# Kernel tuning notes

Measured on AMD Instinct MI355X. Metric: run time of the kernel, lower is better.

Reference implementation:

```python
import jax, jax.numpy as jnp
import numpy as np

N_ITER = 10
TOL = 1e-05
EPS_R = 1e-10
REG = 1e-06
F32_EPS = float(np.finfo(np.float32).eps)


def setup_inputs() -> dict:
    key = jax.random.key(0)
    K, T, F, _ = 6, 2048, 513, 2
    X = jax.random.normal(key, (K, T, F, 2), dtype=jnp.float32)
    return {"X": X}


def _aux_iva_iss(X):
    # X: (K, T, F, 2) real/imag -> complex (F, K, T)
    Xc = (X[..., 0] + 1j * X[..., 1]).astype(jnp.complex64)
    Xc = jnp.transpose(Xc, (2, 0, 1))  # (F, K, T)
    F, K, T = Xc.shape
    eyeK = jnp.eye(K, dtype=jnp.complex64)
    W = jnp.broadcast_to(eyeK, (F, K, K)).astype(jnp.complex64)  # (F, K, K)
    Xh = jnp.conj(Xc)
    done = jnp.array(False)

    for _ in range(N_ITER):
        W_old = W
        # demix: Y[f] = W[f] @ X[f]
        Y = jnp.einsum('fkm,fmt->fkt', W, Xc)
        # per-(source, frame) norms across frequency
        r = jnp.sqrt(jnp.clip(jnp.sum(jnp.abs(Y) ** 2, axis=0), EPS_R))  # (K, T)
        wt = 1.0 / jnp.clip(r, EPS_R)  # laplace contrast g'(r)/r
        # weighted covariances V[f,k] = (X_f * wt[k]) X_f^H / T + reg*I  -> (F, K, K, K)
        V = jnp.einsum('fat,kt,fbt->fkab', Xc, wt.astype(jnp.complex64), Xh) / T
        V = V + REG * eyeK
        # sequential ISS updates over target row k (vectorized over f, m)
        for k in range(K):
            wk = W[:, k, :]  # (F, K)
            wk_c = jnp.conj(wk)
            quad = jnp.einsum('fa,fmab,fb->fm', wk, V, wk_c)  # w_k V_m w_k^H
            denom = jnp.clip(quad.real, EPS_R)  # (F, K)
            num = jnp.einsum('fma,fmab,fb->fm', W, V, wk_c)  # w_m V_m w_k^H
            vk = num / denom  # (F, K)
            vk = vk.at[:, k].set((1.0 - 1.0 / jnp.sqrt(denom[:, k])).astype(jnp.complex64))
            W = W - vk[:, :, None] * wk[:, None, :]
        # emulate early-break on relative change (freeze W once converged)
        W = jnp.where(done, W_old, W)
        diff = jnp.linalg.norm((W - W_old).reshape(-1))
        rel = diff / jnp.clip(jnp.linalg.norm(W_old.reshape(-1)), F32_EPS)
        done = jnp.logical_or(done, rel < TOL)

    Y = jnp.einsum('fkm,fmt->fkt', W, Xc)  # (F, K, T)
    # ref_mic == 0 -> no projection-back rescaling
    Y_out = jnp.transpose(Y, (1, 2, 0))  # (K, T, F)
    return jnp.stack([Y_out.real, Y_out.imag], axis=-1)  # (K, T, F, 2)


def reference(X):
    return _aux_iva_iss(X)
```

## Files before the change

### kernel.cpp

```cpp
#include <hip/hip_runtime.h>
#include <hip/hip_bf16.h>
#include <math.h>

#define T_DIM 2048
#define F_DIM 513
#define N_ITER 10

#define OFF_W0   0
#define OFF_W1   36936
#define OFF_FLG  73872
#define OFF_RA0  73892
#define OFF_RA1  86180
#define OFF_VP   98468

typedef __attribute__((ext_vector_type(8))) short bf16x8;
typedef __attribute__((ext_vector_type(4))) float f32x4;

static __device__ inline unsigned pack2bf(float a, float b) {
    union { __hip_bfloat16 h; unsigned short u; } ca, cb;
    ca.h = __float2bfloat16(a);
    cb.h = __float2bfloat16(b);
    return (unsigned)ca.u | ((unsigned)cb.u << 16);
}

static __device__ inline void scatterV(float* V6, int e, float sum) {
    if (e < 6) {
        V6[(e * 6 + e) * 2]     = sum + 1e-6f;
        V6[(e * 6 + e) * 2 + 1] = 0.f;
    } else if (e < 21) {
        int p = e - 6;
        int a = (p < 1) ? 1 : (p < 3) ? 2 : (p < 6) ? 3 : (p < 10) ? 4 : 5;
        int b = p - a * (a - 1) / 2;
        V6[(a * 6 + b) * 2] = sum;
        V6[(b * 6 + a) * 2] = sum;
    } else {
        int p = e - 21;
        int a = (p < 1) ? 1 : (p < 3) ? 2 : (p < 6) ? 3 : (p < 10) ? 4 : 5;
        int b = p - a * (a - 1) / 2;
        V6[(a * 6 + b) * 2 + 1] =  sum;
        V6[(b * 6 + a) * 2 + 1] = -sum;
    }
}

static __device__ inline bool flag_frozen(const float* flg) {
    float rel = sqrtf(flg[0]) / fmaxf(sqrtf(flg[1]), 1.1920929e-07f);
    return rel < 1e-5f;
}

__global__ __launch_bounds__(256) void transp(const float2* __restrict__ X,
                                              float2* __restrict__ Xt,
                                              float* __restrict__ ws) {
    const int fb  = blockIdx.x + 64 * (blockIdx.y + 17 * blockIdx.z);
    const int tid = threadIdx.x;
    if (fb < 73) {
        int idx = fb * 256 + tid;
        if (idx < F_DIM * 36) {
            int e = idx % 36;
            ws[OFF_W0 + 2 * idx]     = ((e / 6) == (e % 6)) ? 1.0f : 0.0f;
            ws[OFF_W0 + 2 * idx + 1] = 0.0f;
        }
    } else if (fb == 73) {
        if (tid < 20) ws[OFF_FLG + tid] = 0.0f;
    } else if (fb < 122) {
        int idx = (fb - 74) * 256 + tid;
        if (idx < 12288) ws[OFF_RA0 + idx] = 0.0f;
    }

    __shared__ float2 tile[32][33];
    const int k  = blockIdx.z;
    const int t0 = blockIdx.x * 32;
    const int f0 = blockIdx.y * 32;
    const int tx = tid & 31, ty = tid >> 5;
#pragma unroll
    for (int j = 0; j < 4; ++j) {
        int t = t0 + ty + j * 8;
        int f = f0 + tx;
        if (f < F_DIM) tile[ty + j * 8][tx] = X[((size_t)k * T_DIM + t) * F_DIM + f];
    }
    __syncthreads();
#pragma unroll
    for (int j = 0; j < 4; ++j) {
        int f = f0 + ty + j * 8;
        int t = t0 + tx;
        if (f < F_DIM) Xt[((size_t)f * 6 + k) * T_DIM + t] = tile[tx][ty + j * 8];
    }
}

__global__ __launch_bounds__(256) void passA1C(const float2* __restrict__ Xt,
                                               float* __restrict__ ws,
                                               const float* __restrict__ flgIn,
                                               float* __restrict__ flgOut,
                                               const float* __restrict__ wOld,
                                               float* __restrict__ wNew,
                                               float* __restrict__ r2acc,
                                               int do_iss, int gate_en) {
    __shared__ float Wl[16][72];
    __shared__ float VL[16][432];
    const int tid = threadIdx.x, wv = tid >> 6, lane = tid & 63;
    const int tc = blockIdx.x, fc = blockIdx.y;

    const bool frozen = gate_en ? flag_frozen(flgIn) : false;

    const int fl = wv * 4 + (lane >> 4);
    const int f  = fc * 16 + fl;
    const int m  = lane & 15;
    const bool act = (f < F_DIM) && (m < 6);

    if (do_iss == 0) {
        if (act) {
            const float* Wp = wOld + ((size_t)f * 36 + m * 6) * 2;
#pragma unroll
            for (int a = 0; a < 6; ++a) {
                Wl[fl][(m * 6 + a) * 2]     = Wp[2 * a];
                Wl[fl][(m * 6 + a) * 2 + 1] = Wp[2 * a + 1];
            }
        }
    } else if (frozen) {
        if (act) {
            const float* Wp = wOld + ((size_t)f * 36 + m * 6) * 2;
            float* Wq = wNew + ((size_t)f * 36 + m * 6) * 2;
#pragma unroll
            for (int a = 0; a < 6; ++a) {
                Wq[2 * a] = Wp[2 * a]; Wq[2 * a + 1] = Wp[2 * a + 1];
            }
        }
        if (tc == 0 && m == 0 && f < F_DIM) atomicAdd(&flgOut[1], 1.0f);
    } else {
        if (f < F_DIM) {
            const float* vp = ws + OFF_VP + (size_t)f * 4 * 216;
            for (int v = m; v < 216; v += 16) {
                float sum = (vp[v] + vp[216 + v] + vp[432 + v] + vp[648 + v]) * (1.0f / (float)T_DIM);
                scatterV(&VL[fl][(v / 36) * 72], v % 36, sum);
            }
        }
        __syncthreads();
        float w6[6][2], wo6[6][2];
#pragma unroll
        for (int a = 0; a < 6; ++a) { w6[a][0] = 0.f; w6[a][1] = 0.f; wo6[a][0] = 0.f; wo6[a][1] = 0.f; }
        if (act) {
            const float* Wp = wOld + ((size_t)f * 36 + m * 6) * 2;
#pragma unroll
            for (int a = 0; a < 6; ++a) {
                w6[a][0] = Wp[2 * a]; w6[a][1] = Wp[2 * a + 1];
                wo6[a][0] = w6[a][0]; wo6[a][1] = w6[a][1];
            }
        }
        const float2* Vm = (const float2*)&VL[fl][0];
        for (int kk = 0; kk < 6; ++kk) {
            float wk[6][2];
#pragma unroll
            for (int a = 0; a < 6; ++a) {
                wk[a][0] = __shfl(w6[a][0], kk, 16);
                wk[a][1] = __shfl(w6[a][1], kk, 16);
            }
            if (act) {
                float t6[6][2];
#pragma unroll
                for (int a = 0; a < 6; ++a) {
                    float tr = 0.f, ti = 0.f;
#pragma unroll
                    for (int b = 0; b < 6; ++b) {
                        float2 vv = Vm[m * 36 + a * 6 + b];
                        tr += vv.x * wk[b][0] + vv.y * wk[b][1];
                        ti += vv.y * wk[b][0] - vv.x * wk[b][1];
                    }
                    t6[a][0] = tr; t6[a][1] = ti;
                }
                float quad = 0.f, nr = 0.f, ni = 0.f;
#pragma unroll
                for (int a = 0; a < 6; ++a) {
                    quad += wk[a][0] * t6[a][0] - wk[a][1] * t6[a][1];
                    nr   += w6[a][0] * t6[a][0] - w6[a][1] * t6[a][1];
                    ni   += w6[a][0] * t6[a][1] + w6[a][1] * t6[a][0];
                }
                float denom = fmaxf(quad, 1e-10f);
                float vkr, vki;
                if (m == kk) { vkr = 1.0f - 1.0f / sqrtf(denom); vki = 0.0f; }
                else { float inv = 1.0f / denom; vkr = nr * inv; vki = ni * inv; }
#pragma unroll
                for (int a = 0; a < 6; ++a) {
                    w6[a][0] -= vkr * wk[a][0] - vki * wk[a][1];
                    w6[a][1] -= vkr * wk[a][1] + vki * wk[a][0];
                }
            }
        }
        float d2 = 0.f, o2 = 0.f;
        if (act) {
            float* Wq = wNew + ((size_t)f * 36 + m * 6) * 2;
#pragma unroll
            for (int a = 0; a < 6; ++a) {
                Wq[2 * a] = w6[a][0]; Wq[2 * a + 1] = w6[a][1];
                Wl[fl][(m * 6 + a) * 2] = w6[a][0]; Wl[fl][(m * 6 + a) * 2 + 1] = w6[a][1];
                float dr = w6[a][0] - wo6[a][0], di = w6[a][1] - wo6[a][1];
                d2 += dr * dr + di * di;
                o2 += wo6[a][0] * wo6[a][0] + wo6[a][1] * wo6[a][1];
            }
        }
#pragma unroll
        for (int d = 1; d < 8; d <<= 1) {
            d2 += __shfl_xor(d2, d);
            o2 += __shfl_xor(o2, d);
        }
        if (tc == 0 && m == 0 && f < F_DIM) {
            atomicAdd(&flgOut[0], d2);
            atomicAdd(&flgOut[1], o2);
        }
    }
    __syncthreads();
    if (do_iss && frozen) return;

    float* r2s = &VL[0][0];
    const int t2 = tc * 128 + lane * 2;
    float acc[6][2];
#pragma unroll
    for (int k = 0; k < 6; ++k) { acc[k][0] = 0.f; acc[k][1] = 0.f; }
#pragma unroll
    for (int i = 0; i < 4; ++i) {
        const int ff = fc * 16 + wv * 4 + i;
        if (ff < F_DIM) {
            const float2* xf = Xt + (size_t)ff * 6 * T_DIM;
            float4 x4[6];
#pragma unroll
            for (int mm = 0; mm < 6; ++mm)
                x4[mm] = *(const float4*)(xf + (size_t)mm * T_DIM + t2);
            const float* wrow = Wl[wv * 4 + i];
#pragma unroll
            for (int k = 0; k < 6; ++k) {
                float y0r = 0.f, y0i = 0.f, y1r = 0.f, y1i = 0.f;
#pragma unroll
                for (int mm = 0; mm < 6; ++mm) {
                    float wr = wrow[(k * 6 + mm) * 2], wi = wrow[(k * 6 + mm) * 2 + 1];
                    y0r += wr * x4[mm].x - wi * x4[mm].y;
                    y0i += wr * x4[mm].y + wi * x4[mm].x;
                    y1r += wr * x4[mm].z - wi * x4[mm].w;
                    y1i += wr * x4[mm].w + wi * x4[mm].z;
                }
                acc[k][0] += y0r * y0r + y0i * y0i;
                acc[k][1] += y1r * y1r + y1i * y1i;
            }
        }
    }
    __syncthreads();
#pragma unroll
    for (int k = 0; k < 6; ++k) {
        r2s[(wv * 6 + k) * 128 + lane * 2]     = acc[k][0];
        r2s[(wv * 6 + k) * 128 + lane * 2 + 1] = acc[k][1];
    }
    __syncthreads();
    for (int v = tid; v < 768; v += 256) {
        int k = v >> 7, l = v & 127;
        float s = r2s[(0 * 6 + k) * 128 + l] + r2s[(1 * 6 + k) * 128 + l]
                + r2s[(2 * 6 + k) * 128 + l] + r2s[(3 * 6 + k) * 128 + l];
        atomicAdd(&r2acc[k * T_DIM + tc * 128 + l], s);
    }
}

__global__ __launch_bounds__(384) void passB(const float2* __restrict__ Xt,
                                             float* __restrict__ ws,
                                             const float* __restrict__ flgIn,
                                             const float* __restrict__ r2in,
                                             float* __restrict__ r2zero,
                                             int gate_en) {
    __shared__ __align__(16) char plane[16 * 528];
    __shared__ __align__(16) float gbuf[6][256];
    const int tid = threadIdx.x, wv = tid >> 6, lane = tid & 63;
    const int f = blockIdx.x, tq = blockIdx.y;

    if (gate_en && flag_frozen(flgIn)) return;

    {
        int bb = (f * 4 + tq) * 6;
#pragma unroll
        for (int i = 0; i < 6; ++i) {
            int idx = bb + i;
            if (idx < 12288) r2zero[idx] = 0.f;
        }
    }

    const float2* xb = Xt + (size_t)f * 6 * T_DIM;

    for (int i = tid; i < 528; i += 384) ((unsigned*)(plane + 12 * 528))[i] = 0;

    f32x4 acc0 = {0.f, 0.f, 0.f, 0.f};
    f32x4 acc1 = {0.f, 0.f, 0.f, 0.f};
    const int rc = lane & 15;
    const int G  = lane >> 4;
    const char* pu = plane + rc * 528 + G * 16;
    const float* gk = &gbuf[wv][0] + G * 8;

    for (int c = 0; c < 2; ++c) {
        const int t0 = tq * 512 + c * 256;
        __syncthreads();
        for (int i = tid; i < 1536; i += 384) {
            int kk = i >> 8, toff = i & 255;
            float s = r2in[kk * T_DIM + t0 + toff];
            float r = sqrtf(fmaxf(s, 1e-10f));
            gbuf[kk][toff] = 1.0f / fmaxf(r, 1e-10f);
        }
        for (int it = tid; it < 768; it += 384) {
            int mm = it >> 7, q = it & 127;
            float4 xv = *(const float4*)(xb + (size_t)mm * T_DIM + t0 + 2 * q);
            *(unsigned*)(plane + mm * 528 + 4 * q)       = pack2bf(xv.x, xv.z);
            *(unsigned*)(plane + (6 + mm) * 528 + 4 * q) = pack2bf(xv.y, xv.w);
        }
        __syncthreads();
#pragma unroll
        for (int s = 0; s < 8; ++s) {
            bf16x8 b = *(const bf16x8*)(pu + s * 64);
            f32x4 gA = *(const f32x4*)(gk + s * 32);
            f32x4 gB = *(const f32x4*)(gk + s * 32 + 4);
            const unsigned* bu = (const unsigned*)&b;
            bf16x8 a;
            unsigned* au = (unsigned*)&a;
            au[0] = pack2bf(__uint_as_float(bu[0] << 16) * gA[0],
                            __uint_as_float(bu[0] & 0xffff0000u) * gA[1]);
            au[1] = pack2bf(__uint_as_float(bu[1] << 16) * gA[2],
                            __uint_as_float(bu[1] & 0xffff0000u) * gA[3]);
            au[2] = pack2bf(__uint_as_float(bu[2] << 16) * gB[0],
                            __uint_as_float(bu[2] & 0xffff0000u) * gB[1]);
            au[3] = pack2bf(__uint_as_float(bu[3] << 16) * gB[2],
                            __uint_as_float(bu[3] & 0xffff0000u) * gB[3]);
            if (s & 1) acc1 = __builtin_amdgcn_mfma_f32_16x16x32_bf16(a, b, acc1, 0, 0, 0);
            else       acc0 = __builtin_amdgcn_mfma_f32_16x16x32_bf16(a, b, acc0, 0, 0, 0);
        }
    }
    __syncthreads();

    float* S = (float*)plane;
    {
        float* Sk = S + wv * 256;
#pragma unroll
        for (int r = 0; r < 4; ++r)
            Sk[(4 * G + r) * 16 + rc] = acc0[r] + acc1[r];
    }
    __syncthreads();

    if (tid < 216) {
        const int kk = tid / 36, e = tid % 36;
        const float* Sk = S + kk * 256;
        float val;
        if (e < 6) {
            val = Sk[e * 16 + e] + Sk[(6 + e) * 16 + (6 + e)];
        } else if (e < 21) {
            int p = e - 6;
            int a = (p < 1) ? 1 : (p < 3) ? 2 : (p < 6) ? 3 : (p < 10) ? 4 : 5;
            int b = p - a * (a - 1) / 2;
            val = Sk[a * 16 + b] + Sk[(6 + a) * 16 + (6 + b)];
        } else {
            int p = e - 21;
            int a = (p < 1) ? 1 : (p < 3) ? 2 : (p < 6) ? 3 : (p < 10) ? 4 : 5;
            int b = p - a * (a - 1) / 2;
            val = Sk[(6 + a) * 16 + b] - Sk[a * 16 + (6 + b)];
        }
        ws[OFF_VP + ((size_t)f * 4 + tq) * 216 + tid] = val;
    }
}

__global__ __launch_bounds__(64) void passC(float* __restrict__ ws,
                                            const float* __restrict__ flgIn,
                                            const float* __restrict__ wOld,
                                            float* __restrict__ wNew) {
    __shared__ float VL[432];
    const int f = blockIdx.x;
    const int lane = threadIdx.x;
    if (flag_frozen(flgIn)) {
        for (int v = lane; v < 72; v += 64)
            wNew[(size_t)f * 72 + v] = wOld[(size_t)f * 72 + v];
        return;
    }
    {
        const float* vp = ws + OFF_VP + (size_t)f * 4 * 216;
        for (int v = lane; v < 216; v += 64) {
            float sum = (vp[v] + vp[216 + v] + vp[432 + v] + vp[648 + v]) * (1.0f / (float)T_DIM);
            scatterV(&VL[(v / 36) * 72], v % 36, sum);
        }
    }
    __syncthreads();

    const int m = lane;
    const bool act = (m < 6);
    float w6[6][2];
#pragma unroll
    for (int a = 0; a < 6; ++a) { w6[a][0] = 0.f; w6[a][1] = 0.f; }
    if (act) {
        const float* Wp = wOld + ((size_t)f * 36 + m * 6) * 2;
#pragma unroll
        for (int a = 0; a < 6; ++a) {
            w6[a][0] = Wp[2 * a]; w6[a][1] = Wp[2 * a + 1];
        }
    }
    const float2* Vm = (const float2*)VL;
    for (int kk = 0; kk < 6; ++kk) {
        float wk[6][2];
#pragma unroll
        for (int a = 0; a < 6; ++a) {
            wk[a][0] = __shfl(w6[a][0], kk);
            wk[a][1] = __shfl(w6[a][1], kk);
        }
        if (act) {
            float t6[6][2];
#pragma unroll
            for (int a = 0; a < 6; ++a) {
                float tr = 0.f, ti = 0.f;
#pragma unroll
                for (int b = 0; b < 6; ++b) {
                    float2 vv = Vm[m * 36 + a * 6 + b];
                    tr += vv.x * wk[b][0] + vv.y * wk[b][1];
                    ti += vv.y * wk[b][0] - vv.x * wk[b][1];
                }
                t6[a][0] = tr; t6[a][1] = ti;
            }
            float quad = 0.f, nr = 0.f, ni = 0.f;
#pragma unroll
            for (int a = 0; a < 6; ++a) {
                quad += wk[a][0] * t6[a][0] - wk[a][1] * t6[a][1];
                nr   += w6[a][0] * t6[a][0] - w6[a][1] * t6[a][1];
                ni   += w6[a][0] * t6[a][1] + w6[a][1] * t6[a][0];
            }
            float denom = fmaxf(quad, 1e-10f);
            float vkr, vki;
            if (m == kk) { vkr = 1.0f - 1.0f / sqrtf(denom); vki = 0.0f; }
            else { float inv = 1.0f / denom; vkr = nr * inv; vki = ni * inv; }
#pragma unroll
            for (int a = 0; a < 6; ++a) {
                w6[a][0] -= vkr * wk[a][0] - vki * wk[a][1];
                w6[a][1] -= vkr * wk[a][1] + vki * wk[a][0];
            }
        }
    }
    if (act) {
        float* Wq = wNew + ((size_t)f * 36 + m * 6) * 2;
#pragma unroll
        for (int a = 0; a < 6; ++a) {
            Wq[2 * a] = w6[a][0]; Wq[2 * a + 1] = w6[a][1];
        }
    }
}

__global__ __launch_bounds__(256) void finalY(const float2* __restrict__ X,
                                              const float* __restrict__ ws,
                                              float2* __restrict__ out) {
    const int f  = blockIdx.y * 256 + threadIdx.x;
    const int t0 = blockIdx.x * 4;
    if (f >= F_DIM) return;
    const float2* Wf = (const float2*)(ws + OFF_W0) + (size_t)f * 36;
    float2 w[36];
#pragma unroll
    for (int i = 0; i < 36; ++i) w[i] = Wf[i];
#pragma unroll
    for (int tl = 0; tl < 4; ++tl) {
        int t = t0 + tl;
        float2 x[6];
#pragma unroll
        for (int m = 0; m < 6; ++m) x[m] = X[((size_t)m * T_DIM + t) * F_DIM + f];
#pragma unroll
        for (int k = 0; k < 6; ++k) {
            float yr = 0.f, yi = 0.f;
#pragma unroll
            for (int m = 0; m < 6; ++m) {
                float2 wk = w[k * 6 + m];
                yr += wk.x * x[m].x - wk.y * x[m].y;
                yi += wk.x * x[m].y + wk.y * x[m].x;
            }
            out[((size_t)k * T_DIM + t) * F_DIM + f] = make_float2(yr, yi);
        }
    }
}

extern "C" void kernel_launch(void* const* d_in, const int* in_sizes, int n_in,
                              void* d_out, int out_size, void* d_ws, size_t ws_size,
                              hipStream_t stream) {
    (void)in_sizes; (void)n_in; (void)out_size; (void)ws_size;
    const float2* X = (const float2*)d_in[0];
    float* ws = (float*)d_ws;
    float2* out = (float2*)d_out;
    float2* Xt = out;

    float* W[2]  = {ws + OFF_W0,  ws + OFF_W1};
    float* RA[2] = {ws + OFF_RA0, ws + OFF_RA1};
    float* FLG   = ws + OFF_FLG;

    transp<<<dim3(64, 17, 6), 256, 0, stream>>>(X, Xt, ws);
    for (int it = 0; it < N_ITER; ++it) {
        const float* wOld = (it == 0) ? W[0] : W[(it + 1) & 1];
        float* wNew = W[it & 1];
        const float* gIn = (it >= 2) ? FLG + 2 * (it - 2) : FLG;
        float* gOut      = (it >= 1) ? FLG + 2 * (it - 1) : FLG + 18;
        passA1C<<<dim3(16, 33), 256, 0, stream>>>(Xt, ws, gIn, gOut, wOld, wNew,
                                                  RA[it & 1], it > 0, it >= 2);
        const float* gB = (it >= 1) ? FLG + 2 * (it - 1) : FLG;
        passB<<<dim3(F_DIM, 4), 384, 0, stream>>>(Xt, ws, gB,
                                                  RA[it & 1], RA[(it + 1) & 1], it >= 1);
    }
    passC<<<F_DIM, 64, 0, stream>>>(ws, FLG + 16, W[1], W[0]);
    finalY<<<dim3(T_DIM / 4, 3), 256, 0, stream>>>(X, ws, out);
}
```

Measured before the change: 575.2 us.

## Split ISS update out of demix pass into separate per-frequency kernel

Moves the per-frequency ISS update, which each of the 16 time-chunk blocks in the fused kernel computed redundantly, into a separate small kernel with one block per frequency. The demix/norm kernel then only loads the updated W and, with LDS reduced to the W tile and reduction buffer, may fit more blocks per CU. The final ISS pass reuses the same kernel. This removes redundant ISS arithmetic and lowers LDS pressure, at the cost of an extra kernel launch per iteration and a global round trip for W.

```diff
diff --git a/kernel.cpp b/kernel.cpp
--- a/kernel.cpp
+++ b/kernel.cpp
@@ -86,130 +86,123 @@
     }
 }
 
-__global__ __launch_bounds__(256) void passA1C(const float2* __restrict__ Xt,
-                                               float* __restrict__ ws,
-                                               const float* __restrict__ flgIn,
-                                               float* __restrict__ flgOut,
-                                               const float* __restrict__ wOld,
-                                               float* __restrict__ wNew,
-                                               float* __restrict__ r2acc,
-                                               int do_iss, int gate_en) {
+__global__ __launch_bounds__(64) void passI(float* __restrict__ ws,
+                                            const float* __restrict__ flgIn,
+                                            float* __restrict__ flgOut,
+                                            const float* __restrict__ wOld,
+                                            float* __restrict__ wNew,
+                                            int gate_en) {
+    __shared__ float VL[432];
+    const int f = blockIdx.x;
+    const int lane = threadIdx.x;
+    if (gate_en && flag_frozen(flgIn)) {
+        for (int v = lane; v < 72; v += 64)
+            wNew[(size_t)f * 72 + v] = wOld[(size_t)f * 72 + v];
+        if (lane == 0) atomicAdd(&flgOut[1], 1.0f);
+        return;
+    }
+    {
+        const float* vp = ws + OFF_VP + (size_t)f * 4 * 216;
+        for (int v = lane; v < 216; v += 64) {
+            float sum = (vp[v] + vp[216 + v] + vp[432 + v] + vp[648 + v]) * (1.0f / (float)T_DIM);
+            scatterV(&VL[(v / 36) * 72], v % 36, sum);
+        }
+    }
+    __syncthreads();
+
+    const int m = lane;
+    const bool act = (m < 6);
+    float w6[6][2], wo6[6][2];
+#pragma unroll
+    for (int a = 0; a < 6; ++a) { w6[a][0] = 0.f; w6[a][1] = 0.f; wo6[a][0] = 0.f; wo6[a][1] = 0.f; }
+    if (act) {
+        const float* Wp = wOld + ((size_t)f * 36 + m * 6) * 2;
+#pragma unroll
+        for (int a = 0; a < 6; ++a) {
+            w6[a][0] = Wp[2 * a]; w6[a][1] = Wp[2 * a + 1];
+            wo6[a][0] = w6[a][0]; wo6[a][1] = w6[a][1];
+        }
+    }
+    const float2* Vm = (const float2*)VL;
+    for (int kk = 0; kk < 6; ++kk) {
+        float wk[6][2];
+#pragma unroll
+        for (int a = 0; a < 6; ++a) {
+            wk[a][0] = __shfl(w6[a][0], kk);
+            wk[a][1] = __shfl(w6[a][1], kk);
+        }
+        if (act) {
+            float t6[6][2];
+#pragma unroll
+            for (int a = 0; a < 6; ++a) {
+                float tr = 0.f, ti = 0.f;
+#pragma unroll
+                for (int b = 0; b < 6; ++b) {
+                    float2 vv = Vm[m * 36 + a * 6 + b];
+                    tr += vv.x * wk[b][0] + vv.y * wk[b][1];
+                    ti += vv.y * wk[b][0] - vv.x * wk[b][1];
+                }
+                t6[a][0] = tr; t6[a][1] = ti;
+            }
+            float quad = 0.f, nr = 0.f, ni = 0.f;
+#pragma unroll
+            for (int a = 0; a < 6; ++a) {
+                quad += wk[a][0] * t6[a][0] - wk[a][1] * t6[a][1];
+                nr   += w6[a][0] * t6[a][0] - w6[a][1] * t6[a][1];
+                ni   += w6[a][0] * t6[a][1] + w6[a][1] * t6[a][0];
+            }
+            float denom = fmaxf(quad, 1e-10f);
+            float vkr, vki;
+            if (m == kk) { vkr = 1.0f - 1.0f / sqrtf(denom); vki = 0.0f; }
+            else { float inv = 1.0f / denom; vkr = nr * inv; vki = ni * inv; }
+#pragma unroll
+            for (int a = 0; a < 6; ++a) {
+                w6[a][0] -= vkr * wk[a][0] - vki * wk[a][1];
+                w6[a][1] -= vkr * wk[a][1] + vki * wk[a][0];
+            }
+        }
+    }
+    float d2 = 0.f, o2 = 0.f;
+    if (act) {
+        float* Wq = wNew + ((size_t)f * 36 + m * 6) * 2;
+#pragma unroll
+        for (int a = 0; a < 6; ++a) {
+            Wq[2 * a] = w6[a][0]; Wq[2 * a + 1] = w6[a][1];
+            float dr = w6[a][0] - wo6[a][0], di = w6[a][1] - wo6[a][1];
+            d2 += dr * dr + di * di;
+            o2 += wo6[a][0] * wo6[a][0] + wo6[a][1] * wo6[a][1];
+        }
+    }
+#pragma unroll
+    for (int d = 1; d < 8; d <<= 1) {
+        d2 += __shfl_xor(d2, d);
+        o2 += __shfl_xor(o2, d);
+    }
+    if (lane == 0) {
+        atomicAdd(&flgOut[0], d2);
+        atomicAdd(&flgOut[1], o2);
+    }
+}
+
+__global__ __launch_bounds__(256) void passA(const float2* __restrict__ Xt,
+                                             const float* __restrict__ Wcur,
+                                             float* __restrict__ r2acc,
+                                             const float* __restrict__ flgIn,
+                                             int gate_en) {
     __shared__ float Wl[16][72];
-    __shared__ float VL[16][432];
+    __shared__ float r2s[4][6][128];
     const int tid = threadIdx.x, wv = tid >> 6, lane = tid & 63;
     const int tc = blockIdx.x, fc = blockIdx.y;
 
-    const bool frozen = gate_en ? flag_frozen(flgIn) : false;
-
-    const int fl = wv * 4 + (lane >> 4);
-    const int f  = fc * 16 + fl;
-    const int m  = lane & 15;
-    const bool act = (f < F_DIM) && (m < 6);
-
-    if (do_iss == 0) {
-        if (act) {
-            const float* Wp = wOld + ((size_t)f * 36 + m * 6) * 2;
-#pragma unroll
-            for (int a = 0; a < 6; ++a) {
-                Wl[fl][(m * 6 + a) * 2]     = Wp[2 * a];
-                Wl[fl][(m * 6 + a) * 2 + 1] = Wp[2 * a + 1];
-            }
-        }
-    } else if (frozen) {
-        if (act) {
-            const float* Wp = wOld + ((size_t)f * 36 + m * 6) * 2;
-            float* Wq = wNew + ((size_t)f * 36 + m * 6) * 2;
-#pragma unroll
-            for (int a = 0; a < 6; ++a) {
-                Wq[2 * a] = Wp[2 * a]; Wq[2 * a + 1] = Wp[2 * a + 1];
-            }
-        }
-        if (tc == 0 && m == 0 && f < F_DIM) atomicAdd(&flgOut[1], 1.0f);
-    } else {
-        if (f < F_DIM) {
-            const float* vp = ws + OFF_VP + (size_t)f * 4 * 216;
-            for (int v = m; v < 216; v += 16) {
-                float sum = (vp[v] + vp[216 + v] + vp[432 + v] + vp[648 + v]) * (1.0f / (float)T_DIM);
-                scatterV(&VL[fl][(v / 36) * 72], v % 36, sum);
-            }
-        }
-        __syncthreads();
-        float w6[6][2], wo6[6][2];
-#pragma unroll
-        for (int a = 0; a < 6; ++a) { w6[a][0] = 0.f; w6[a][1] = 0.f; wo6[a][0] = 0.f; wo6[a][1] = 0.f; }
-        if (act) {
-            const float* Wp = wOld + ((size_t)f * 36 + m * 6) * 2;
-#pragma unroll
-            for (int a = 0; a < 6; ++a) {
-                w6[a][0] = Wp[2 * a]; w6[a][1] = Wp[2 * a + 1];
-                wo6[a][0] = w6[a][0]; wo6[a][1] = w6[a][1];
-            }
-        }
-        const float2* Vm = (const float2*)&VL[fl][0];
-        for (int kk = 0; kk < 6; ++kk) {
-            float wk[6][2];
-#pragma unroll
-            for (int a = 0; a < 6; ++a) {
-                wk[a][0] = __shfl(w6[a][0], kk, 16);
-                wk[a][1] = __shfl(w6[a][1], kk, 16);
-            }
-            if (act) {
-                float t6[6][2];
-#pragma unroll
-                for (int a = 0; a < 6; ++a) {
-                    float tr = 0.f, ti = 0.f;
-#pragma unroll
-                    for (int b = 0; b < 6; ++b) {
-                        float2 vv = Vm[m * 36 + a * 6 + b];
-                        tr += vv.x * wk[b][0] + vv.y * wk[b][1];
-                        ti += vv.y * wk[b][0] - vv.x * wk[b][1];
-                    }
-                    t6[a][0] = tr; t6[a][1] = ti;
-                }
-                float quad = 0.f, nr = 0.f, ni = 0.f;
-#pragma unroll
-                for (int a = 0; a < 6; ++a) {
-                    quad += wk[a][0] * t6[a][0] - wk[a][1] * t6[a][1];
-                    nr   += w6[a][0] * t6[a][0] - w6[a][1] * t6[a][1];
-                    ni   += w6[a][0] * t6[a][1] + w6[a][1] * t6[a][0];
-                }
-                float denom = fmaxf(quad, 1e-10f);
-                float vkr, vki;
-                if (m == kk) { vkr = 1.0f - 1.0f / sqrtf(denom); vki = 0.0f; }
-                else { float inv = 1.0f / denom; vkr = nr * inv; vki = ni * inv; }
-#pragma unroll
-                for (int a = 0; a < 6; ++a) {
-                    w6[a][0] -= vkr * wk[a][0] - vki * wk[a][1];
-                    w6[a][1] -= vkr * wk[a][1] + vki * wk[a][0];
-                }
-            }
-        }
-        float d2 = 0.f, o2 = 0.f;
-        if (act) {
-            float* Wq = wNew + ((size_t)f * 36 + m * 6) * 2;
-#pragma unroll
-            for (int a = 0; a < 6; ++a) {
-                Wq[2 * a] = w6[a][0]; Wq[2 * a + 1] = w6[a][1];
-                Wl[fl][(m * 6 + a) * 2] = w6[a][0]; Wl[fl][(m * 6 + a) * 2 + 1] = w6[a][1];
-                float dr = w6[a][0] - wo6[a][0], di = w6[a][1] - wo6[a][1];
-                d2 += dr * dr + di * di;
-                o2 += wo6[a][0] * wo6[a][0] + wo6[a][1] * wo6[a][1];
-            }
-        }
-#pragma unroll
-        for (int d = 1; d < 8; d <<= 1) {
-            d2 += __shfl_xor(d2, d);
-            o2 += __shfl_xor(o2, d);
-        }
-        if (tc == 0 && m == 0 && f < F_DIM) {
-            atomicAdd(&flgOut[0], d2);
-            atomicAdd(&flgOut[1], o2);
-        }
-    }
-    __syncthreads();
-    if (do_iss && frozen) return;
-
-    float* r2s = &VL[0][0];
+    if (gate_en && flag_frozen(flgIn)) return;
+
+    for (int idx = tid; idx < 16 * 72; idx += 256) {
+        int fl = idx / 72, e = idx % 72;
+        int ff = fc * 16 + fl;
+        Wl[fl][e] = (ff < F_DIM) ? Wcur[(size_t)ff * 72 + e] : 0.f;
+    }
+    __syncthreads();
+
     const int t2 = tc * 128 + lane * 2;
     float acc[6][2];
 #pragma unroll
@@ -240,17 +233,15 @@
             }
         }
     }
-    __syncthreads();
 #pragma unroll
     for (int k = 0; k < 6; ++k) {
-        r2s[(wv * 6 + k) * 128 + lane * 2]     = acc[k][0];
-        r2s[(wv * 6 + k) * 128 + lane * 2 + 1] = acc[k][1];
+        r2s[wv][k][lane * 2]     = acc[k][0];
+        r2s[wv][k][lane * 2 + 1] = acc[k][1];
     }
     __syncthreads();
     for (int v = tid; v < 768; v += 256) {
         int k = v >> 7, l = v & 127;
-        float s = r2s[(0 * 6 + k) * 128 + l] + r2s[(1 * 6 + k) * 128 + l]
-                + r2s[(2 * 6 + k) * 128 + l] + r2s[(3 * 6 + k) * 128 + l];
+        float s = r2s[0][k][l] + r2s[1][k][l] + r2s[2][k][l] + r2s[3][k][l];
         atomicAdd(&r2acc[k * T_DIM + tc * 128 + l], s);
     }
 }
@@ -356,87 +347,6 @@
     }
 }
 
-__global__ __launch_bounds__(64) void passC(float* __restrict__ ws,
-                                            const float* __restrict__ flgIn,
-                                            const float* __restrict__ wOld,
-                                            float* __restrict__ wNew) {
-    __shared__ float VL[432];
-    const int f = blockIdx.x;
-    const int lane = threadIdx.x;
-    if (flag_frozen(flgIn)) {
-        for (int v = lane; v < 72; v += 64)
-            wNew[(size_t)f * 72 + v] = wOld[(size_t)f * 72 + v];
-        return;
-    }
-    {
-        const float* vp = ws + OFF_VP + (size_t)f * 4 * 216;
-        for (int v = lane; v < 216; v += 64) {
-            float sum = (vp[v] + vp[216 + v] + vp[432 + v] + vp[648 + v]) * (1.0f / (float)T_DIM);
-            scatterV(&VL[(v / 36) * 72], v % 36, sum);
-        }
-    }
-    __syncthreads();
-
-    const int m = lane;
-    const bool act = (m < 6);
-    float w6[6][2];
-#pragma unroll
-    for (int a = 0; a < 6; ++a) { w6[a][0] = 0.f; w6[a][1] = 0.f; }
-    if (act) {
-        const float* Wp = wOld + ((size_t)f * 36 + m * 6) * 2;
-#pragma unroll
-        for (int a = 0; a < 6; ++a) {
-            w6[a][0] = Wp[2 * a]; w6[a][1] = Wp[2 * a + 1];
-        }
-    }
-    const float2* Vm = (const float2*)VL;
-    for (int kk = 0; kk < 6; ++kk) {
-        float wk[6][2];
-#pragma unroll
-        for (int a = 0; a < 6; ++a) {
-            wk[a][0] = __shfl(w6[a][0], kk);
-            wk[a][1] = __shfl(w6[a][1], kk);
-        }
-        if (act) {
-            float t6[6][2];
-#pragma unroll
-            for (int a = 0; a < 6; ++a) {
-                float tr = 0.f, ti = 0.f;
-#pragma unroll
-                for (int b = 0; b < 6; ++b) {
-                    float2 vv = Vm[m * 36 + a * 6 + b];
-                    tr += vv.x * wk[b][0] + vv.y * wk[b][1];
-                    ti += vv.y * wk[b][0] - vv.x * wk[b][1];
-                }
-                t6[a][0] = tr; t6[a][1] = ti;
-            }
-            float quad = 0.f, nr = 0.f, ni = 0.f;
-#pragma unroll
-            for (int a = 0; a < 6; ++a) {
-                quad += wk[a][0] * t6[a][0] - wk[a][1] * t6[a][1];
-                nr   += w6[a][0] * t6[a][0] - w6[a][1] * t6[a][1];
-                ni   += w6[a][0] * t6[a][1] + w6[a][1] * t6[a][0];
-            }
-            float denom = fmaxf(quad, 1e-10f);
-            float vkr, vki;
-            if (m == kk) { vkr = 1.0f - 1.0f / sqrtf(denom); vki = 0.0f; }
-            else { float inv = 1.0f / denom; vkr = nr * inv; vki = ni * inv; }
-#pragma unroll
-            for (int a = 0; a < 6; ++a) {
-                w6[a][0] -= vkr * wk[a][0] - vki * wk[a][1];
-                w6[a][1] -= vkr * wk[a][1] + vki * wk[a][0];
-            }
-        }
-    }
-    if (act) {
-        float* Wq = wNew + ((size_t)f * 36 + m * 6) * 2;
-#pragma unroll
-        for (int a = 0; a < 6; ++a) {
-            Wq[2 * a] = w6[a][0]; Wq[2 * a + 1] = w6[a][1];
-        }
-    }
-}
-
 __global__ __launch_bounds__(256) void finalY(const float2* __restrict__ X,
                                               const float* __restrict__ ws,
                                               float2* __restrict__ out) {
@@ -484,14 +394,16 @@
     for (int it = 0; it < N_ITER; ++it) {
         const float* wOld = (it == 0) ? W[0] : W[(it + 1) & 1];
         float* wNew = W[it & 1];
-        const float* gIn = (it >= 2) ? FLG + 2 * (it - 2) : FLG;
-        float* gOut      = (it >= 1) ? FLG + 2 * (it - 1) : FLG + 18;
-        passA1C<<<dim3(16, 33), 256, 0, stream>>>(Xt, ws, gIn, gOut, wOld, wNew,
-                                                  RA[it & 1], it > 0, it >= 2);
-        const float* gB = (it >= 1) ? FLG + 2 * (it - 1) : FLG;
-        passB<<<dim3(F_DIM, 4), 384, 0, stream>>>(Xt, ws, gB,
+        if (it >= 1) {
+            const float* gIn = (it >= 2) ? FLG + 2 * (it - 2) : FLG;
+            passI<<<F_DIM, 64, 0, stream>>>(ws, gIn, FLG + 2 * (it - 1),
+                                            wOld, wNew, it >= 2);
+        }
+        const float* gA = (it >= 1) ? FLG + 2 * (it - 1) : FLG;
+        passA<<<dim3(16, 33), 256, 0, stream>>>(Xt, wNew, RA[it & 1], gA, it >= 1);
+        passB<<<dim3(F_DIM, 4), 384, 0, stream>>>(Xt, ws, gA,
                                                   RA[it & 1], RA[(it + 1) & 1], it >= 1);
     }
-    passC<<<F_DIM, 64, 0, stream>>>(ws, FLG + 16, W[1], W[0]);
+    passI<<<F_DIM, 64, 0, stream>>>(ws, FLG + 16, FLG + 18, W[1], W[0], 1);
     finalY<<<dim3(T_DIM / 4, 3), 256, 0, stream>>>(X, ws, out);
 }
```

Measured after the change: 669.9 us. +16.5%, slower.
